# Optimization experiments

Measured on AMD Instinct MI355X. Metric: run time of the kernel, lower is better.

The kernel has to match this reference:

```python
import jax, jax.numpy as jnp
import numpy as np

NB_KNN = (10, 20, 100, 200)   # values of k to evaluate; max_k = 200
T = 0.07                       # softmax temperature
NUM_CLASSES = 1000


def setup_inputs() -> dict:
    key = jax.random.key(0)
    k1, k2, k3 = jax.random.split(key, 3)
    features_rank = jax.random.normal(k1, (256, 512), jnp.float32)      # (B, d) query features
    train_features = jax.random.normal(k2, (100000, 512), jnp.float32)  # (N, d) train bank
    train_labels = jax.random.randint(k3, (100000,), 0, NUM_CLASSES)     # (N,) int labels
    return {"features_rank": features_rank, "train_features": train_features,
            "train_labels": train_labels}


def _knn_probs(features_rank, train_features, train_labels):
    max_k = max(NB_KNN)
    # similarity: (B, N) = (B, d) @ (d, N)  -- mirrors torch.mm(broadcasted, train_features_rank_T)
    sims = features_rank @ train_features.T
    topk_sims, idx = jax.lax.top_k(sims, max_k)          # (B, max_k), sorted descending
    neighbors = train_labels[idx]                         # (B, max_k) gathered labels
    w = jax.nn.softmax(topk_sims / T, axis=1)             # (B, max_k) neighbor weights
    B = features_rank.shape[0]
    rows = jnp.arange(B)[:, None]                         # (B, 1) row indices for scatter
    # Instead of materializing one_hot (B, max_k, C) and summing prefixes,
    # scatter-add the first k weights into per-class buckets (same math, fused).
    probs = [jnp.zeros((B, NUM_CLASSES), w.dtype).at[rows, neighbors[:, :k]].add(w[:, :k])
             for k in NB_KNN]
    return jnp.stack(probs, axis=0)                       # (len(NB_KNN), B, C)


def reference(features_rank, train_features, train_labels):
    return _knn_probs(features_rank, train_features, train_labels)
```

## Files before the change

### kernel.cpp

```cpp
#include <hip/hip_runtime.h>
#include <math.h>

#define KDIM   512
#define NCLS   1000
#define CUTOFF 3.0f
#define MAXCAP 4096
#define BN     64
#define BK     64
#define NSTAGE (KDIM / BK)
#define FCAP   512

typedef __attribute__((ext_vector_type(8))) short  short8;
typedef __attribute__((ext_vector_type(4))) float  floatx4;

__device__ __forceinline__ unsigned enc_f(float f) {
    unsigned u = __float_as_uint(f);
    return (u & 0x80000000u) ? ~u : (u | 0x80000000u);
}
__device__ __forceinline__ float dec_f(unsigned k) {
    unsigned u = (k & 0x80000000u) ? (k & 0x7FFFFFFFu) : ~k;
    return __uint_as_float(u);
}
__device__ __forceinline__ unsigned short f2bf(float f) {
    unsigned u = __float_as_uint(f);
    u += 0x7FFFu + ((u >> 16) & 1u);
    return (unsigned short)(u >> 16);
}
__device__ __forceinline__ float bf2f(unsigned short h) {
    return __uint_as_float(((unsigned)h) << 16);
}

__device__ __forceinline__ void bar_nodrain() {
    __builtin_amdgcn_sched_barrier(0);
    asm volatile("s_waitcnt lgkmcnt(0)");
    __builtin_amdgcn_s_barrier();
    __builtin_amdgcn_sched_barrier(0);
}

__global__ void k_prep(const float* __restrict__ A, unsigned short* __restrict__ af,
                       unsigned* __restrict__ cnt, unsigned* __restrict__ gmax, int Brows) {
    int t = blockIdx.x * blockDim.x + threadIdx.x;
    if (t < Brows) { cnt[t] = 0u; gmax[t] = enc_f(-3.0e38f); }
    if (t >= Brows * (KDIM / 8)) return;
    int r = t >> 6;
    int o = t & 63;
    int s16 = r >> 4, c = o >> 2, kq = o & 3;
    int lane = kq * 16 + (r & 15);
    const float* src = A + (size_t)r * KDIM + o * 8;
    size_t bhi = ((size_t)((s16 * 16 + c) * 2 + 0) * 64 + lane) * 8;
    size_t blo = ((size_t)((s16 * 16 + c) * 2 + 1) * 64 + lane) * 8;
#pragma unroll
    for (int j = 0; j < 8; ++j) {
        float f = src[j];
        unsigned short h = f2bf(f);
        af[bhi + j] = h;
        af[blo + j] = f2bf(f - bf2f(h));
    }
}

__global__ __launch_bounds__(512, 4) void k_gemm(
    const float* __restrict__ Bt,
    const unsigned short* __restrict__ af,
    float* __restrict__ cand_val, int* __restrict__ cand_idx,
    unsigned* __restrict__ cnt, unsigned* __restrict__ gmax,
    int N, int cap)
{
    __shared__ short8 BsH[2][512];
    __shared__ short8 BsL[2][512];

    const int tid  = threadIdx.x;
    const int lane = tid & 63;
    const int wid  = tid >> 6;
    const int colBase = blockIdx.x * BN;

    const int nl  = tid >> 3;
    const int k8  = (tid & 7) * 8;
    const int gcol = colBase + nl;
    const bool colok = (gcol < N);
    const float* bsrc = Bt + (size_t)gcol * KDIM + k8;
    const int chw = k8 >> 5;
    const int kqw = (k8 >> 3) & 3;
    const int ctw = (nl >> 4) & 3;
    const int fidw = chw * 4 + ctw;
    const int lfw  = kqw * 16 + (nl & 15);
    const int slotw = fidw * 64 + (lfw ^ (kqw * 2 + chw));

    floatx4 acc[2][4];
#pragma unroll
    for (int rt = 0; rt < 2; ++rt)
#pragma unroll
        for (int ct = 0; ct < 4; ++ct)
            acc[rt][ct] = (floatx4){0.f, 0.f, 0.f, 0.f};

    const float4 z4 = make_float4(0.f, 0.f, 0.f, 0.f);
    float4 c0 = colok ? *(const float4*)(bsrc)          : z4;
    float4 c1 = colok ? *(const float4*)(bsrc + 4)      : z4;
    float4 n0 = colok ? *(const float4*)(bsrc + BK)     : z4;
    float4 n1 = colok ? *(const float4*)(bsrc + BK + 4) : z4;

    {
        union { float4 v[2]; float f[8]; } P;
        union { short8 v; unsigned short u[8]; } H, L;
        P.v[0] = c0; P.v[1] = c1;
#pragma unroll
        for (int j = 0; j < 8; ++j) {
            unsigned short h = f2bf(P.f[j]);
            H.u[j] = h; L.u[j] = f2bf(P.f[j] - bf2f(h));
        }
        BsH[0][slotw] = H.v; BsL[0][slotw] = L.v;
    }
    bar_nodrain();

    for (int s = 0; s < NSTAGE; ++s) {
        short8 aH[2][2], aL[2][2];
#pragma unroll
        for (int chunk = 0; chunk < 2; ++chunk) {
            const int cg = s * 2 + chunk;
#pragma unroll
            for (int rt = 0; rt < 2; ++rt) {
                const int s16 = wid * 2 + rt;
                size_t sl = (size_t)((s16 * 16 + cg) * 2) * 64 + lane;
                aH[chunk][rt] = *(const short8*)(af + sl * 8);
                aL[chunk][rt] = *(const short8*)(af + (sl + 64) * 8);
            }
        }
        __builtin_amdgcn_sched_barrier(0);

        if (s + 1 < NSTAGE) {
            c0 = n0; c1 = n1;
            if (s + 2 < NSTAGE) {
                const float* p = bsrc + (s + 2) * BK;
                n0 = colok ? *(const float4*)(p)     : z4;
                n1 = colok ? *(const float4*)(p + 4) : z4;
            }
            union { float4 v[2]; float f[8]; } P;
            union { short8 v; unsigned short u[8]; } H, L;
            P.v[0] = c0; P.v[1] = c1;
#pragma unroll
            for (int j = 0; j < 8; ++j) {
                unsigned short h = f2bf(P.f[j]);
                H.u[j] = h; L.u[j] = f2bf(P.f[j] - bf2f(h));
            }
            BsH[(s + 1) & 1][slotw] = H.v; BsL[(s + 1) & 1][slotw] = L.v;
        }

        __builtin_amdgcn_s_setprio(1);
#pragma unroll
        for (int chunk = 0; chunk < 2; ++chunk) {
            const int g = (lane >> 4) * 2 + chunk;
#pragma unroll
            for (int ct = 0; ct < 4; ++ct) {
                const int idx = (chunk * 4 + ct) * 64 + (lane ^ g);
                short8 bh = BsH[s & 1][idx];
                short8 bl = BsL[s & 1][idx];
#pragma unroll
                for (int rt = 0; rt < 2; ++rt) {
                    acc[rt][ct] = __builtin_amdgcn_mfma_f32_16x16x32_bf16(aH[chunk][rt], bh, acc[rt][ct], 0, 0, 0);
                    acc[rt][ct] = __builtin_amdgcn_mfma_f32_16x16x32_bf16(aH[chunk][rt], bl, acc[rt][ct], 0, 0, 0);
                    acc[rt][ct] = __builtin_amdgcn_mfma_f32_16x16x32_bf16(aL[chunk][rt], bh, acc[rt][ct], 0, 0, 0);
                }
            }
        }
        __builtin_amdgcn_s_setprio(0);

        bar_nodrain();
    }

    const int q   = lane >> 4;
    const int n15 = lane & 15;
#pragma unroll
    for (int rt = 0; rt < 2; ++rt) {
#pragma unroll
        for (int reg = 0; reg < 4; ++reg) {
            const int row = wid * 32 + rt * 16 + q * 4 + reg;
            float m = fmaxf(fmaxf(acc[rt][0][reg], acc[rt][1][reg]),
                            fmaxf(acc[rt][2][reg], acc[rt][3][reg]));
#pragma unroll
            for (int off = 1; off < 16; off <<= 1) m = fmaxf(m, __shfl_xor(m, off));
            unsigned oldk = 0u;
            if (n15 == 0) oldk = atomicMax(&gmax[row], enc_f(m));
            oldk = (unsigned)__shfl((int)oldk, lane & 48);
            const float thr = fmaxf(dec_f(oldk), m) - CUTOFF;
#pragma unroll
            for (int ct = 0; ct < 4; ++ct) {
                const float v = acc[rt][ct][reg];
                const int col = colBase + ct * 16 + n15;
                if (v >= thr && col < N) {
                    unsigned p = atomicAdd(&cnt[row], 1u);
                    if (p < (unsigned)cap) {
                        cand_val[(size_t)row * cap + p] = v;
                        cand_idx[(size_t)row * cap + p] = col;
                    }
                }
            }
        }
    }
}

__global__ __launch_bounds__(256) void k_finalize(
    const float* __restrict__ cand_val,
    const int* __restrict__ cand_idx,
    const unsigned* __restrict__ cnt,
    const unsigned* __restrict__ gmax,
    const int* __restrict__ labels,
    float* __restrict__ out,
    int Brows, int cap)
{
    __shared__ float s_val[FCAP];
    __shared__ int   s_idx[FCAP];
    __shared__ float s_out[4 * NCLS];
    __shared__ int   s_n;
    __shared__ float s_part[4];
    __shared__ float s_Z;

    const int row = blockIdx.x;
    const int tid = threadIdx.x;
    if (tid == 0) s_n = 0;
    __syncthreads();

    const float m   = dec_f(gmax[row]);
    const float thr = m - CUTOFF;
    const int n = min((int)cnt[row], cap);
    for (int i = tid; i < n; i += 256) {
        float v = cand_val[(size_t)row * cap + i];
        if (v >= thr) {
            int p = atomicAdd(&s_n, 1);
            if (p < FCAP) { s_val[p] = v; s_idx[p] = cand_idx[(size_t)row * cap + i]; }
        }
    }
    for (int c = tid; c < 4 * NCLS; c += 256) s_out[c] = 0.f;
    __syncthreads();
    const int ns = min(s_n, FCAP);

    float e0 = 0.f, e1 = 0.f;
    int   r0 = 0x7fffffff, r1 = 0x7fffffff;
    int   lab0 = 0, lab1 = 0;
    if (tid < ns) {
        const float v = s_val[tid]; const int ix = s_idx[tid];
        int rk = 0;
        for (int j = 0; j < ns; ++j) {
            const float vj = s_val[j];
            rk += (vj > v || (vj == v && s_idx[j] < ix)) ? 1 : 0;
        }
        r0 = rk;
        if (rk < 200) { e0 = expf((v - m) * (1.0f / 0.07f)); lab0 = labels[ix]; }
    }
    if (tid + 256 < ns) {
        const int i2 = tid + 256;
        const float v = s_val[i2]; const int ix = s_idx[i2];
        int rk = 0;
        for (int j = 0; j < ns; ++j) {
            const float vj = s_val[j];
            rk += (vj > v || (vj == v && s_idx[j] < ix)) ? 1 : 0;
        }
        r1 = rk;
        if (rk < 200) { e1 = expf((v - m) * (1.0f / 0.07f)); lab1 = labels[ix]; }
    }

    float part = e0 + e1;
#pragma unroll
    for (int off = 32; off >= 1; off >>= 1) part += __shfl_down(part, off);
    if ((tid & 63) == 0) s_part[tid >> 6] = part;
    __syncthreads();
    if (tid == 0) s_Z = (s_part[0] + s_part[1]) + (s_part[2] + s_part[3]);
    __syncthreads();
    const float invZ = 1.0f / s_Z;

    if (r0 < 200) {
        const float w = e0 * invZ;
        if (r0 < 10)  atomicAdd(&s_out[0 * NCLS + lab0], w);
        if (r0 < 20)  atomicAdd(&s_out[1 * NCLS + lab0], w);
        if (r0 < 100) atomicAdd(&s_out[2 * NCLS + lab0], w);
        atomicAdd(&s_out[3 * NCLS + lab0], w);
    }
    if (r1 < 200) {
        const float w = e1 * invZ;
        if (r1 < 10)  atomicAdd(&s_out[0 * NCLS + lab1], w);
        if (r1 < 20)  atomicAdd(&s_out[1 * NCLS + lab1], w);
        if (r1 < 100) atomicAdd(&s_out[2 * NCLS + lab1], w);
        atomicAdd(&s_out[3 * NCLS + lab1], w);
    }
    __syncthreads();

    for (int c = tid; c < 4 * NCLS; c += 256) {
        const int sl = c / NCLS, cc = c - sl * NCLS;
        out[(size_t)sl * ((size_t)Brows * NCLS) + (size_t)row * NCLS + cc] = s_out[c];
    }
}

extern "C" void kernel_launch(void* const* d_in, const int* in_sizes, int n_in,
                              void* d_out, int out_size, void* d_ws, size_t ws_size,
                              hipStream_t stream) {
    const float* A      = (const float*)d_in[0];
    const float* Bt     = (const float*)d_in[1];
    const int*   labels = (const int*)d_in[2];
    float* out = (float*)d_out;

    const int Brows = in_sizes[0] / KDIM;
    const int N     = in_sizes[2];

    size_t af_elems = (size_t)Brows * KDIM * 2;
    unsigned short* af = (unsigned short*)d_ws;
    unsigned* cnt  = (unsigned*)(af + af_elems);
    unsigned* gmax = cnt + Brows;
    char* rest = (char*)(gmax + Brows);
    size_t used  = (size_t)(rest - (char*)d_ws);
    size_t avail = (ws_size > used) ? (ws_size - used) : 0;
    int cap = (int)((avail / ((size_t)Brows * 8)) < (size_t)MAXCAP
                        ? (avail / ((size_t)Brows * 8)) : (size_t)MAXCAP);
    if (cap < 1) cap = 1;
    float* cand_val = (float*)rest;
    int*   cand_idx = (int*)(cand_val + (size_t)Brows * cap);

    k_prep<<<(Brows * (KDIM / 8) + 255) / 256, 256, 0, stream>>>(A, af, cnt, gmax, Brows);
    k_gemm<<<(N + BN - 1) / BN, 512, 0, stream>>>(Bt, af, cand_val, cand_idx, cnt, gmax, N, cap);
    k_finalize<<<Brows, 256, 0, stream>>>(cand_val, cand_idx, cnt, gmax, labels, out, Brows, cap);
}
```

Before: 399.3 us.

## Seed per-row max from sampled columns, tighten cutoff, deepen B prefetch

Adds a k_seed kernel that computes exact dot products against 128 strided train columns per query row and seeds the global running max, so candidate filtering in the GEMM rejects more columns from the start. The candidate cutoff margin is tightened from 3.0 to 1.0 below the running max, which shrinks the candidate buffers and the finalize work. The GEMM's global B prefetch is deepened from two stages to three with a rotating register ring and a fully unrolled stage loop. The tighter cutoff can drop true top-200 neighbours if the score spread near the top exceeds the margin, and the extra prefetch registers may lower occupancy.

```diff
diff --git a/kernel.cpp b/kernel.cpp
--- a/kernel.cpp
+++ b/kernel.cpp
@@ -3,7 +3,7 @@
 
 #define KDIM   512
 #define NCLS   1000
-#define CUTOFF 3.0f
+#define CUTOFF 1.0f
 #define MAXCAP 4096
 #define BN     64
 #define BK     64
@@ -58,6 +58,34 @@
     }
 }
 
+__global__ __launch_bounds__(256) void k_seed(
+    const float* __restrict__ A, const float* __restrict__ Bt,
+    unsigned* __restrict__ gmax, int N)
+{
+    __shared__ float arow[KDIM];
+    const int r = blockIdx.x, t = threadIdx.x;
+    for (int i = t; i < KDIM; i += 256) arow[i] = A[(size_t)r * KDIM + i];
+    __syncthreads();
+    const int lane = t & 63, wid = t >> 6;
+    float best = -3.0e38f;
+    const int stride = N >> 7;
+#pragma unroll
+    for (int s = 0; s < 32; ++s) {
+        int j = wid * 32 + s;
+        long col = (long)j * stride;
+        const float* b = Bt + col * KDIM + lane * 8;
+        float4 x0 = *(const float4*)(b);
+        float4 x1 = *(const float4*)(b + 4);
+        const float* a = arow + lane * 8;
+        float d = x0.x*a[0] + x0.y*a[1] + x0.z*a[2] + x0.w*a[3]
+                + x1.x*a[4] + x1.y*a[5] + x1.z*a[6] + x1.w*a[7];
+#pragma unroll
+        for (int off = 32; off >= 1; off >>= 1) d += __shfl_xor(d, off);
+        best = fmaxf(best, d);
+    }
+    if (lane == 0) atomicMax(&gmax[r], enc_f(best));
+}
+
 __global__ __launch_bounds__(512, 4) void k_gemm(
     const float* __restrict__ Bt,
     const unsigned short* __restrict__ af,
@@ -93,12 +121,15 @@
             acc[rt][ct] = (floatx4){0.f, 0.f, 0.f, 0.f};
 
     const float4 z4 = make_float4(0.f, 0.f, 0.f, 0.f);
-    float4 c0 = colok ? *(const float4*)(bsrc)          : z4;
-    float4 c1 = colok ? *(const float4*)(bsrc + 4)      : z4;
-    float4 n0 = colok ? *(const float4*)(bsrc + BK)     : z4;
-    float4 n1 = colok ? *(const float4*)(bsrc + BK + 4) : z4;
-
+
+    float4 rgA[3], rgB[3];
     {
+        float4 c0 = colok ? *(const float4*)(bsrc)     : z4;
+        float4 c1 = colok ? *(const float4*)(bsrc + 4) : z4;
+        rgA[1] = colok ? *(const float4*)(bsrc + 1 * BK)     : z4;
+        rgB[1] = colok ? *(const float4*)(bsrc + 1 * BK + 4) : z4;
+        rgA[2] = colok ? *(const float4*)(bsrc + 2 * BK)     : z4;
+        rgB[2] = colok ? *(const float4*)(bsrc + 2 * BK + 4) : z4;
         union { float4 v[2]; float f[8]; } P;
         union { short8 v; unsigned short u[8]; } H, L;
         P.v[0] = c0; P.v[1] = c1;
@@ -111,6 +142,7 @@
     }
     bar_nodrain();
 
+#pragma unroll
     for (int s = 0; s < NSTAGE; ++s) {
         short8 aH[2][2], aL[2][2];
 #pragma unroll
@@ -126,16 +158,17 @@
         }
         __builtin_amdgcn_sched_barrier(0);
 
+        if (s + 3 < NSTAGE) {
+            const float* p = bsrc + (s + 3) * BK;
+            rgA[(s + 3) % 3] = colok ? *(const float4*)(p)     : z4;
+            rgB[(s + 3) % 3] = colok ? *(const float4*)(p + 4) : z4;
+        }
+        __builtin_amdgcn_sched_barrier(0);
+
         if (s + 1 < NSTAGE) {
-            c0 = n0; c1 = n1;
-            if (s + 2 < NSTAGE) {
-                const float* p = bsrc + (s + 2) * BK;
-                n0 = colok ? *(const float4*)(p)     : z4;
-                n1 = colok ? *(const float4*)(p + 4) : z4;
-            }
             union { float4 v[2]; float f[8]; } P;
             union { short8 v; unsigned short u[8]; } H, L;
-            P.v[0] = c0; P.v[1] = c1;
+            P.v[0] = rgA[(s + 1) % 3]; P.v[1] = rgB[(s + 1) % 3];
 #pragma unroll
             for (int j = 0; j < 8; ++j) {
                 unsigned short h = f2bf(P.f[j]);
@@ -313,6 +346,7 @@
     int*   cand_idx = (int*)(cand_val + (size_t)Brows * cap);
 
     k_prep<<<(Brows * (KDIM / 8) + 255) / 256, 256, 0, stream>>>(A, af, cnt, gmax, Brows);
+    k_seed<<<Brows, 256, 0, stream>>>(A, Bt, gmax, N);
     k_gemm<<<(N + BN - 1) / BN, 512, 0, stream>>>(Bt, af, cand_val, cand_idx, cnt, gmax, N, cap);
     k_finalize<<<Brows, 256, 0, stream>>>(cand_val, cand_idx, cnt, gmax, labels, out, Brows, cap);
 }
```

After: 427.1 us. 7.0% more time.
